# Kernel tuning notes

Measured on AMD Instinct MI355X. Metric: run time of the kernel, lower is better.

## Reference

```python
import jax, jax.numpy as jnp
import numpy as np

B, F, HU, HC = 8192, 100, 128, 512


def _lin(key, din, dout, bias=True, scale=0.02):
    k1, k2 = jax.random.split(key)
    w = jax.random.normal(k1, (din, dout), jnp.float32) * scale
    if bias:
        b = jax.random.normal(k2, (dout,), jnp.float32) * scale
        return w, b
    return (w,)


def setup_inputs() -> dict:
    key = jax.random.key(0)
    ks = jax.random.split(key, 24)
    d = {}
    d['feature_list'] = jax.random.normal(ks[0], (B, F), jnp.float32)
    d['is_treat'] = jax.random.uniform(ks[1], (B,), jnp.float32)
    d['emb'] = jax.random.normal(ks[2], (F, HU), jnp.float32) * 0.02
    d['t_w'], d['t_b'] = _lin(ks[3], 1, HU)
    d['qw'], d['qb'] = _lin(ks[4], HU, HU)
    d['kw'], d['kb'] = _lin(ks[5], HU, HU)
    d['vw'], d['vb'] = _lin(ks[6], HU, HU)
    (d['a1w'],) = _lin(ks[7], HU, HU, bias=False)
    d['a2w'], d['a2b'] = _lin(ks[8], HU, HU)
    (d['a3w'],) = _lin(ks[9], HU, 1, bias=False)
    d['c1w'], d['c1b'] = _lin(ks[10], F * HU, HC)
    d['c2w'], d['c2b'] = _lin(ks[11], HC, HC)
    d['c3w'], d['c3b'] = _lin(ks[12], HC, HC // 2)
    d['c4w'], d['c4b'] = _lin(ks[13], HC // 2, HC // 4)
    d['c5w'], d['c5b'] = _lin(ks[14], HC // 4, HC // 8)
    d['clw'], d['clb'] = _lin(ks[15], HC // 8, 1)
    d['ctw'], d['ctb'] = _lin(ks[16], HC // 8, 1)
    d['u1w'], d['u1b'] = _lin(ks[17], HU, HU)
    d['u2w'], d['u2b'] = _lin(ks[18], HU, HU // 2)
    d['u3w'], d['u3b'] = _lin(ks[19], HU // 2, HU // 4)
    d['u4w'], d['u4b'] = _lin(ks[20], HU // 4, HU // 8)
    d['tlw'], d['tlb'] = _lin(ks[21], HU // 8, 1)
    d['utw'], d['utb'] = _lin(ks[22], HU // 8, 1)
    return d


def reference(feature_list, is_treat, emb, t_w, t_b, qw, qb, kw, kb, vw, vb,
              a1w, a2w, a2b, a3w, c1w, c1b, c2w, c2b, c3w, c3b, c4w, c4b,
              c5w, c5b, clw, clb, ctw, ctb, u1w, u1b, u2w, u2b, u3w, u3b,
              u4w, u4b, tlw, tlb, utw, utb):
    elu = jax.nn.elu
    sig = jax.nn.sigmoid
    b, f = feature_list.shape
    h = emb.shape[1]
    # per-feature embedding: [B, F, H]
    x_rep = feature_list[:, :, None] * emb[None, :, :]
    # normalize over the feature axis (dim=1), as in torch.linalg.norm(dim=1)
    nx = x_rep / jnp.linalg.norm(x_rep, axis=1, keepdims=True)
    # self-attention with sigmoid-then-softmax scores
    Q = nx @ qw + qb
    K = nx @ kw + kb
    V = nx @ vw + vb
    scores = jnp.einsum('bfh,bgh->bfg', Q, K) / (h ** 0.5)
    attn_w = jax.nn.softmax(sig(scores), axis=-1)
    xx = jnp.einsum('bfg,bgh->bfh', attn_w, V).reshape(b, f * h)
    # control net tower
    c = elu(xx @ c1w + c1b)
    c = elu(c @ c2w + c2b)
    c = elu(c @ c3w + c3b)
    c = elu(c @ c4w + c4b)
    c = elu(c @ c5w + c5b)  # is_self=True
    c_logit = c @ clw + clb
    c_tau = c @ ctw + ctb
    c_prob = sig(c_logit)
    # treatment representation: Linear(1, hu) on ones -> [B, H]
    t_rep = jnp.ones((b, 1), feature_list.dtype) @ t_w.reshape(1, h) + t_b
    # interaction attention (vectorized over features)
    att = jax.nn.relu(sig(t_rep @ a1w)[:, None, :] + sig(x_rep @ a2w + a2b))
    att = (att @ a3w)[..., 0]  # [B, F]
    attn = jax.nn.softmax(att, axis=1)
    xt = jnp.einsum('bf,bfh->bh', attn, x_rep)
    # uplift net tower
    u = elu(xt @ u1w + u1b)
    u = elu(u @ u2w + u2b)
    u = elu(u @ u3w + u3b)
    u = elu(u @ u4w + u4b)  # is_self=True
    t_logit = u @ tlw + tlb
    u_tau = u @ utw + utb
    t_prob = sig(t_logit)
    return (c_logit, c_prob, c_tau, t_logit, t_prob, u_tau)
```

## Files before the change

### kernel.cpp

```cpp
#include <hip/hip_runtime.h>
#include <hip/hip_bf16.h>

typedef __bf16 bf16;
typedef __bf16 bf16x8 __attribute__((ext_vector_type(8)));
typedef __bf16 bf16x4 __attribute__((ext_vector_type(4)));
typedef float f32x4 __attribute__((ext_vector_type(4)));
typedef unsigned u32x4 __attribute__((ext_vector_type(4)));

#define DEVI static __device__ __forceinline__

DEVI float sigmoidf_(float x){ return 1.0f/(1.0f+__expf(-x)); }
DEVI float eluf_(float x){ return x>0.f ? x : (__expf(x)-1.f); }
DEVI f32x4 mfma16(bf16x8 a, bf16x8 b, f32x4 c){ return __builtin_amdgcn_mfma_f32_16x16x32_bf16(a,b,c,0,0,0); }
DEVI f32x4 mfma8(long a, long b, f32x4 c){ return __builtin_amdgcn_mfma_f32_16x16x32_fp8_fp8(a,b,c,0,0,0); }
DEVI unsigned pack2_(float a, float b){
    union { bf16 v[2]; unsigned u; } t; t.v[0]=(bf16)a; t.v[1]=(bf16)b; return t.u;
}
DEVI unsigned long long pack4_(float a, float b, float c, float d){
    union { bf16 v[4]; unsigned long long u; } t;
    t.v[0]=(bf16)a; t.v[1]=(bf16)b; t.v[2]=(bf16)c; t.v[3]=(bf16)d; return t.u;
}
DEVI unsigned cvtfp8x4_(float a, float b, float c, float d){
    int v = __builtin_amdgcn_cvt_pk_fp8_f32(a, b, 0, false);
    v = __builtin_amdgcn_cvt_pk_fp8_f32(c, d, v, true);
    return (unsigned)v;
}
DEVI void gld16_(const void* g, void* l){
    __builtin_amdgcn_global_load_lds((const __attribute__((address_space(1))) void*)g,
                                     (__attribute__((address_space(3))) void*)l, 16, 0, 0);
}

#define B_ 8192
#define F_ 100
#define FP 112
#define H_ 128
#define KC_ 12800
#define SPLIT_ 4
#define FP8SC 16.0f

#define SWZ(r,bc) ((bc) ^ (((r)&7)<<4))
DEVI int swzk_(int row, int k){ return (k & ~127) | ((k & 127) ^ ((row&7)<<4)); }

DEVI void dotrans_(float (*t)[33], const float* in, bf16* out, int R, int C, int bx, int by, int tid){
    int c0 = bx*32, r0 = by*32;
    int tc = tid & 31, tr = tid >> 5;
    #pragma unroll
    for (int i=0;i<4;i++){
        int r = tr + i*8;
        t[r][tc] = in[(size_t)(r0+r)*C + c0 + tc];
    }
    __syncthreads();
    #pragma unroll
    for (int i=0;i<4;i++){
        int ro = tr + i*8;
        out[(size_t)(c0+ro)*R + r0 + tc] = (bf16)t[tc][ro];
    }
}

DEVI void dotrans_swz_(float (*t)[33], const float* in, bf16* out, int R, int C, int bx, int by, int tid){
    int c0 = bx*32, r0 = by*32;
    int tc = tid & 31, tr = tid >> 5;
    #pragma unroll
    for (int i=0;i<4;i++){
        int r = tr + i*8;
        t[r][tc] = in[(size_t)(r0+r)*C + c0 + tc];
    }
    __syncthreads();
    #pragma unroll
    for (int i=0;i<4;i++){
        int ro = tr + i*8;
        int n = c0+ro;
        int ob = swzk_(n, (r0+tc)*2);
        *(bf16*)((char*)out + (size_t)n*R*2 + ob) = (bf16)t[tc][ro];
    }
}

__global__ void k_prep_all(const float* __restrict__ qw, const float* __restrict__ qb,
                           const float* __restrict__ kw, const float* __restrict__ kb,
                           const float* __restrict__ tw, const float* __restrict__ tb,
                           const float* __restrict__ a1w, const float* __restrict__ vw,
                           const float* __restrict__ a2w, const float* __restrict__ c2w,
                           const float* __restrict__ c3w,
                           bf16* __restrict__ mextT, float* __restrict__ sigt, float* __restrict__ cconst,
                           bf16* __restrict__ wvT, bf16* __restrict__ wa2t,
                           bf16* __restrict__ c2wt, bf16* __restrict__ c3wt){
    __shared__ float t[32][33];
    const float rsc = 0.08838834764831845f;
    int blk = blockIdx.x, tid = threadIdx.x;
    if (blk < 9){
        #pragma unroll 1
        for (int e=0; e<8; ++e){
            int idx = e*256 + tid;
            int n = blk*16 + (idx>>7), h = idx&127;
            float acc = 0.f;
            if (n < 128){
                for (int d=0; d<128; ++d) acc += qw[h*128+d]*kw[n*128+d];
            } else if (n == 128){
                for (int d=0; d<128; ++d) acc += qw[h*128+d]*kb[d];
            } else if (n == 129){
                for (int d=0; d<128; ++d) acc += kw[h*128+d]*qb[d];
            }
            mextT[n*128+h] = (bf16)(acc*rsc);
        }
    } else if (blk == 9){
        if (tid < 128){
            float acc = 0.f;
            for (int h=0; h<128; ++h) acc += (tw[h]+tb[h]) * a1w[h*128+tid];
            sigt[tid] = sigmoidf_(acc);
        } else if (tid == 128){
            float acc = 0.f;
            for (int d=0; d<128; ++d) acc += qb[d]*kb[d];
            cconst[0] = acc*rsc;
        }
    } else if (blk < 26){
        int i = blk-10; dotrans_(t, vw, wvT, 128,128, i&3, i>>2, tid);
    } else if (blk < 42){
        int i = blk-26; dotrans_(t, a2w, wa2t, 128,128, i&3, i>>2, tid);
    } else if (blk < 298){
        int i = blk-42; dotrans_swz_(t, c2w, c2wt, 512,512, i&15, i>>4, tid);
    } else {
        int i = blk-298; dotrans_swz_(t, c3w, c3wt, 512,256, i&7, i>>3, tid);
    }
}

DEVI int kappa_(int k){
    int f = k>>7, h = k&127;
    if (f < 96)
        return (((f>>4)<<3) | (h>>4))*256 + ((f&15)>>2)*64 + (h&15)*4 + (f&3);
    else
        return 12288 + (h>>4)*64 + (h&15)*4 + (f&3);
}

__global__ __launch_bounds__(256,2) void k_gk(
    const float* __restrict__ c1w, unsigned char* __restrict__ c1wtk8,
    const float* __restrict__ feat, const float* __restrict__ emb,
    const bf16* __restrict__ wa2t, const float* __restrict__ a2b,
    const float* __restrict__ a3w, const float* __restrict__ sigt,
    float* __restrict__ attg)
{
    __shared__ char A[37888];
    int blk = blockIdx.x, tid = threadIdx.x;
    if (blk < 6400){
        float (*t)[33] = (float(*)[33])A;
        const int C = 512;
        int c0 = (blk&15)*32, r0 = (blk>>4)*32;
        int tc = tid & 31, tr = tid >> 5;
        #pragma unroll
        for (int i=0;i<4;i++){
            int r = tr + i*8;
            t[r][tc] = c1w[(size_t)(r0+r)*C + c0 + tc];
        }
        __syncthreads();
        #pragma unroll
        for (int i=0;i<4;i++){
            int ro = tr + i*8;
            float x = t[tc][ro]*FP8SC;
            int v = __builtin_amdgcn_cvt_pk_fp8_f32(x, x, 0, false);
            int n = c0+ro;
            c1wtk8[(size_t)n*KC_ + swzk_(n, kappa_(r0+tc))] = (unsigned char)v;
        }
        return;
    }
    bf16 (*sAt)[72] = (bf16(*)[72])A;
    bf16 (*sBt)[72] = (bf16(*)[72])(A + 18432);
    float (*sRed)[128] = (float(*)[128])(A + 36864);
    int w=tid>>6, lane=tid&63, l15=lane&15, l4=lane>>4;
    int m0 = (blk-6400)*128;
    int wr = w>>1, wc = w&1;
    f32x4 acc[4][4];
    #pragma unroll
    for(int mi=0;mi<4;mi++)
        #pragma unroll
        for(int ni=0;ni<4;ni++) acc[mi][ni] = (f32x4){0.f,0.f,0.f,0.f};

    #pragma unroll 1
    for (int k0=0; k0<128; k0+=64){
        __syncthreads();
        #pragma unroll
        for (int t4=0; t4<4; t4++){
            int t = tid + t4*256;
            int row=t>>3, col=(t&7)*8;
            int gr = m0+row;
            int bb = gr/112, ff = gr - bb*112;
            bf16x8 o;
            if (ff < F_){
                float fv = feat[(size_t)bb*F_ + ff];
                const float* ep = emb + ff*H_ + k0 + col;
                f32x4 e0 = *(const f32x4*)ep;
                f32x4 e1 = *(const f32x4*)(ep+4);
                o[0]=(bf16)(fv*e0[0]); o[1]=(bf16)(fv*e0[1]); o[2]=(bf16)(fv*e0[2]); o[3]=(bf16)(fv*e0[3]);
                o[4]=(bf16)(fv*e1[0]); o[5]=(bf16)(fv*e1[1]); o[6]=(bf16)(fv*e1[2]); o[7]=(bf16)(fv*e1[3]);
            } else {
                #pragma unroll
                for (int e=0;e<8;e++) o[e]=(bf16)0.f;
            }
            *(bf16x8*)&sAt[row][col] = o;
            *(bf16x8*)&sBt[row][col] = *(const bf16x8*)(wa2t + row*H_ + k0 + col);
        }
        __syncthreads();
        #pragma unroll
        for(int ks=0;ks<2;ks++){
            bf16x8 af[4], bfr[4];
            #pragma unroll
            for(int mi=0;mi<4;mi++) af[mi] = *(const bf16x8*)&sAt[wr*64+mi*16+l15][ks*32+l4*8];
            #pragma unroll
            for(int ni=0;ni<4;ni++) bfr[ni] = *(const bf16x8*)&sBt[wc*64+ni*16+l15][ks*32+l4*8];
            #pragma unroll
            for(int mi=0;mi<4;mi++)
                #pragma unroll
                for(int ni=0;ni<4;ni++)
                    acc[mi][ni] = mfma16(af[mi], bfr[ni], acc[mi][ni]);
        }
    }
    float sg[4], ab[4], a3[4];
    #pragma unroll
    for (int ni=0;ni<4;ni++){
        int n = wc*64 + ni*16 + l15;
        sg[ni]=sigt[n]; ab[ni]=a2b[n]; a3[ni]=a3w[n];
    }
    #pragma unroll
    for (int mi=0;mi<4;mi++){
        float sj[4] = {0.f,0.f,0.f,0.f};
        #pragma unroll
        for (int ni=0;ni<4;ni++){
            #pragma unroll
            for (int j=0;j<4;j++){
                float u = sigmoidf_(acc[mi][ni][j] + ab[ni]);
                float t = sg[ni] + u;
                t = t>0.f ? t : 0.f;
                sj[j] += t*a3[ni];
            }
        }
        #pragma unroll
        for (int j=0;j<4;j++){
            float v = sj[j];
            #pragma unroll
            for (int m=1;m<16;m<<=1) v += __shfl_xor(v,m,16);
            sj[j]=v;
        }
        if (l15==0){
            #pragma unroll
            for (int j=0;j<4;j++) sRed[wc][wr*64+mi*16+l4*4+j] = sj[j];
        }
    }
    __syncthreads();
    if (tid < 128) attg[(size_t)m0 + tid] = sRed[0][tid] + sRed[1][tid];
}

__global__ __launch_bounds__(512,2) void k_attn2(
    const float* __restrict__ feat, const float* __restrict__ emb,
    const bf16* __restrict__ mextT, const bf16* __restrict__ wvT,
    const float* __restrict__ vb, const float* __restrict__ cconst,
    const float* __restrict__ attg,
    unsigned char* __restrict__ xxb, bf16* __restrict__ xtb)
{
    __shared__ char L[81792];
    char* Lm = L;
    char* Ln = L + 32768;
    float* sFeat  = (float*)(L+61440);
    float* normP  = (float*)(L+62336);
    float* sAw    = (float*)(L+77568);
    float* sNorm  = (float*)(L+79872);
    float* sAlpha = (float*)(L+80384);
    float* sBeta  = (float*)(L+80832);
    float* sInv   = (float*)(L+81280);

    int b = blockIdx.x;
    int tid = threadIdx.x, w = tid>>6, lane = tid&63;
    int l15 = lane&15, l4 = lane>>4;
    bf16 (*sP)[72] = (bf16(*)[72])(L + 61440 + w*2304);

    bf16x8 awv[4];
    #pragma unroll
    for (int kc=0;kc<4;kc++)
        awv[kc] = *(const bf16x8*)(wvT + (w*16+l15)*H_ + kc*32 + l4*8);
    float vbr = vb[w*16+l15];

    #pragma unroll 2
    for (int v = tid; v < 128*16; v += 512){
        int n = v >> 4, cg = (v & 15) * 8;
        *(u32x4*)(Lm + n*256 + SWZ(n, cg*2)) = *(const u32x4*)(mextT + n*128 + cg);
    }
    if (tid < FP) sFeat[tid] = (tid<F_) ? feat[(size_t)b*F_+tid] : 0.f;
    if (w==0){
        const float* ag = attg + (size_t)b*FP;
        float a0 = (lane<F_)? ag[lane] : -1e30f;
        float a1 = (lane+64<F_)? ag[lane+64] : -1e30f;
        float m = fmaxf(a0,a1);
        #pragma unroll
        for(int s=1;s<64;s<<=1) m = fmaxf(m, __shfl_xor(m,s,64));
        float e0 = (lane<F_)? __expf(a0-m):0.f;
        float e1 = (lane+64<F_)? __expf(a1-m):0.f;
        float s = e0+e1;
        #pragma unroll
        for(int t=1;t<64;t<<=1) s += __shfl_xor(s,t,64);
        float inv = 1.f/s;
        if (lane<FP) sAw[lane] = e0*inv;
        if (lane+64<FP) sAw[lane+64] = e1*inv;
    }
    __syncthreads();

    int hp = (tid&63)*2, gg = tid>>6;
    {
        float fa0=0.f, fa1=0.f;
        #pragma unroll 4
        for (int it=0; it<13; ++it){
            int f = gg + 8*it;
            if (f < F_){
                float2 e2 = *(const float2*)(emb + f*H_ + hp);
                float v0 = sFeat[f]*e2.x, v1 = sFeat[f]*e2.y;
                fa0 += v0*v0; fa1 += v1*v1;
            }
        }
        *(float2*)(normP + gg*128 + hp) = make_float2(fa0, fa1);
    }
    __syncthreads();
    if (tid < 128){
        float s = 0.f;
        #pragma unroll
        for (int g2=0; g2<8; ++g2) s += normP[g2*128 + tid];
        sNorm[tid] = sqrtf(s);
    }
    __syncthreads();

    {
        float rn0 = __builtin_amdgcn_rcpf(sNorm[hp]);
        float rn1 = __builtin_amdgcn_rcpf(sNorm[hp+1]);
        #pragma unroll 4
        for (int it=0; it<13; ++it){
            int f = gg + 8*it;
            if (f < F_){
                float2 e2 = *(const float2*)(emb + f*H_ + hp);
                *(unsigned*)(Ln + f*256 + SWZ(f, hp*2)) = pack2_(sFeat[f]*e2.x*rn0, sFeat[f]*e2.y*rn1);
            }
        }
        for (int z=tid; z<768; z+=512){
            int f = 100 + (z>>6), hz = (z&63)*2;
            *(unsigned*)(Ln + f*256 + SWZ(f, hz*2)) = 0u;
        }
    }
    __syncthreads();

    int mt = w;

    if (mt < 7){
        bf16x8 bfr8[4];
        #pragma unroll
        for (int kc=0;kc<4;kc++)
            bfr8[kc] = *(const bf16x8*)(mextT + (128+(l15&1))*H_ + kc*32 + l4*8);
        f32x4 acc = {0.f,0.f,0.f,0.f};
        #pragma unroll
        for (int kc=0;kc<4;kc++){
            bf16x8 a = *(const bf16x8*)(Ln + (mt*16+l15)*256 + SWZ(mt*16+l15, (kc*32+l4*8)*2));
            acc = mfma16(a, bfr8[kc], acc);
        }
        if (l15==0){
            #pragma unroll
            for (int j=0;j<4;j++) sAlpha[mt*16+l4*4+j] = acc[j];
        }
        if (l15==1){
            #pragma unroll
            for (int j=0;j<4;j++) sBeta[mt*16+l4*4+j] = acc[j];
        }
    }
    __syncthreads();

    const float cc = cconst[0];
    unsigned long long uexB[3];
    if (mt < 7){
        bf16x8 afxi[4];
        #pragma unroll
        for (int kc=0;kc<4;kc++)
            afxi[kc] = *(const bf16x8*)(Ln + (mt*16+l15)*256 + SWZ(mt*16+l15, (kc*32+l4*8)*2));
        f32x4 sc[7];
        #pragma unroll
        for (int gt=0; gt<7; gt++) sc[gt] = (f32x4){0.f,0.f,0.f,0.f};
        #pragma unroll 1
        for (int p=0; p<2; p++){
            #pragma unroll 2
            for (int nt4=0; nt4<4; nt4++){
                int nt = p*4 + nt4;
                bf16x8 bw[4];
                #pragma unroll
                for (int kc=0;kc<4;kc++)
                    bw[kc] = *(const bf16x8*)(Lm + (nt*16+l15)*256 + SWZ(nt*16+l15, (kc*32+l4*8)*2));
                f32x4 d = {0.f,0.f,0.f,0.f};
                #pragma unroll
                for (int kc=0;kc<4;kc++) d = mfma16(bw[kc], afxi[kc], d);
                *(unsigned long long*)(&sP[l15][nt4*16 + l4*4]) = pack4_(d[0],d[1],d[2],d[3]);
            }
            bf16x8 afs0 = *(const bf16x8*)&sP[l15][l4*8];
            bf16x8 afs1 = *(const bf16x8*)&sP[l15][32+l4*8];
            #pragma unroll
            for (int gt=0; gt<7; gt++){
                int r = gt*16+l15;
                bf16x8 b0 = *(const bf16x8*)(Ln + r*256 + SWZ(r, (p*64 + l4*8)*2));
                bf16x8 b1 = *(const bf16x8*)(Ln + r*256 + SWZ(r, (p*64 + 32 + l4*8)*2));
                sc[gt] = mfma16(b0, afs0, sc[gt]);
                sc[gt] = mfma16(b1, afs1, sc[gt]);
            }
        }
        float aj = sAlpha[mt*16+l15];
        float rs = 0.f;
        #pragma unroll
        for (int gt=0; gt<7; gt++){
            f32x4 bt4 = *(const f32x4*)&sBeta[gt*16+l4*4];
            float e[4];
            #pragma unroll
            for (int j=0;j<4;j++){
                int g = gt*16 + l4*4 + j;
                float val = sc[gt][j] + aj + bt4[j] + cc;
                e[j] = (g<F_) ? __expf(sigmoidf_(val)) : 0.f;
                rs += e[j];
            }
            if (gt < 4)
                *(unsigned long long*)(&sP[l15][gt*16 + l4*4]) = pack4_(e[0],e[1],e[2],e[3]);
            else
                uexB[gt-4] = pack4_(e[0],e[1],e[2],e[3]);
        }
        rs += __shfl_xor(rs, 16, 64);
        rs += __shfl_xor(rs, 32, 64);
        if (l4 == 0) sInv[w*16 + l15] = 1.f/rs;
    } else {
        int h = lane;
        float a0=0.f, a1=0.f;
        #pragma unroll 4
        for (int f=0; f<F_; ++f){
            float awf = sAw[f];
            a0 += awf * (float)*(const bf16*)(Ln + f*256 + SWZ(f, h*2));
            a1 += awf * (float)*(const bf16*)(Ln + f*256 + SWZ(f, (h+64)*2));
        }
        xtb[(size_t)b*H_ + h]      = (bf16)(a0 * sNorm[h]);
        xtb[(size_t)b*H_ + h + 64] = (bf16)(a1 * sNorm[h+64]);
    }

    unsigned long long vpku[7];
    #pragma unroll
    for (int gt=0; gt<7; gt++){
        f32x4 acc = {0.f,0.f,0.f,0.f};
        #pragma unroll
        for (int kc=0;kc<4;kc++){
            int r = gt*16+l15;
            bf16x8 a = *(const bf16x8*)(Ln + r*256 + SWZ(r, (kc*32+l4*8)*2));
            acc = mfma16(a, awv[kc], acc);
        }
        vpku[gt] = pack4_(acc[0]+vbr, acc[1]+vbr, acc[2]+vbr, acc[3]+vbr);
    }
    __syncthreads();

    {
        int hrow = w*16 + l15;
        #pragma unroll
        for (int gt=0; gt<7; gt++)
            *(unsigned long long*)(Lm + hrow*256 + SWZ(hrow, gt*32 + l4*8)) = vpku[gt];
    }
    __syncthreads();

    if (mt < 7){
        bf16x8 ap0 = *(const bf16x8*)&sP[l15][l4*8];
        bf16x8 ap1 = *(const bf16x8*)&sP[l15][32+l4*8];
        f32x4 acc8[8];
        #pragma unroll
        for (int ht=0;ht<8;ht++) acc8[ht] = (f32x4){0.f,0.f,0.f,0.f};
        #pragma unroll
        for (int ht=0; ht<8; ht++){
            int r = ht*16+l15;
            bf16x8 bv0 = *(const bf16x8*)(Lm + r*256 + SWZ(r, (l4*8)*2));
            bf16x8 bv1 = *(const bf16x8*)(Lm + r*256 + SWZ(r, (32+l4*8)*2));
            acc8[ht] = mfma16(ap0, bv0, acc8[ht]);
            acc8[ht] = mfma16(ap1, bv1, acc8[ht]);
        }
        #pragma unroll
        for (int gt=4; gt<7; gt++)
            *(unsigned long long*)(&sP[l15][(gt-4)*16 + l4*4]) = uexB[gt-4];
        *(unsigned long long*)(&sP[l15][48 + l4*4]) = 0ull;
        bf16x8 ap2 = *(const bf16x8*)&sP[l15][l4*8];
        bf16x8 ap3 = *(const bf16x8*)&sP[l15][32+l4*8];
        #pragma unroll
        for (int ht=0; ht<8; ht++){
            int r = ht*16+l15;
            int c2 = 64+l4*8;
            int c3 = 96+l4*8;  if (c3 >= 112) c3 = 96;
            bf16x8 bv2 = *(const bf16x8*)(Lm + r*256 + SWZ(r, c2*2));
            bf16x8 bv3 = *(const bf16x8*)(Lm + r*256 + SWZ(r, c3*2));
            acc8[ht] = mfma16(ap2, bv2, acc8[ht]);
            acc8[ht] = mfma16(ap3, bv3, acc8[ht]);
        }
        float fs[4];
        #pragma unroll
        for (int j=0;j<4;j++) fs[j] = sInv[w*16 + l4*4 + j] * FP8SC;
        #pragma unroll
        for (int ht=0; ht<8; ht++){
            unsigned u = cvtfp8x4_(acc8[ht][0]*fs[0], acc8[ht][1]*fs[1], acc8[ht][2]*fs[2], acc8[ht][3]*fs[3]);
            if (mt < 6){
                *(unsigned*)(xxb + (size_t)b*KC_ + swzk_(b, (mt*8+ht)*256 + lane*4)) = u;
            } else if (l4 == 0){
                *(unsigned*)(xxb + (size_t)b*KC_ + swzk_(b, 12288 + ht*64 + l15*4)) = u;
            }
        }
    }
}

__global__ __launch_bounds__(512,2) void k_gemm_fp8(const unsigned char* __restrict__ A,
        const unsigned char* __restrict__ Bt, bf16* __restrict__ part, int M, int N, int K, int KS)
{
    __shared__ unsigned char S[49152];
    int tid=threadIdx.x, w=tid>>6, lane=tid&63, l15=lane&15, l4=lane>>4;
    int m0 = blockIdx.y*128, n0 = blockIdx.x*256;
    int kbeg = blockIdx.z*KS, kend = kbeg + KS;
    int wr = w>>2, wc = w&3;
    int offW = w*1024 + lane*16;
    int rS = offW >> 7, cS = offW & 127;
    f32x4 acc[4][4];
    #pragma unroll
    for(int mi=0;mi<4;mi++)
        #pragma unroll
        for(int ni=0;ni<4;ni++) acc[mi][ni] = (f32x4){0.f,0.f,0.f,0.f};

    int sx = (l15&7)<<4;

    for (int k0=kbeg; k0<kend; k0+=128){
        __syncthreads();
        gld16_(A + (size_t)(m0 + rS     )*K + k0 + cS, S + offW);
        gld16_(A + (size_t)(m0 + rS + 64)*K + k0 + cS, S + offW + 8192);
        #pragma unroll
        for (int q=0;q<4;q++)
            gld16_(Bt + (size_t)(n0 + q*64 + rS)*K + k0 + cS, S + 16384 + q*8192 + offW);
        __syncthreads();
        #pragma unroll
        for(int ks=0;ks<4;ks++){
            int co = (ks*32 + l4*8) ^ sx;
            long af[4], bfr[4];
            #pragma unroll
            for(int mi=0;mi<4;mi++) af[mi] = *(const long*)(S + (wr*64+mi*16+l15)*128 + co);
            #pragma unroll
            for(int ni=0;ni<4;ni++) bfr[ni] = *(const long*)(S + 16384 + (wc*64+ni*16+l15)*128 + co);
            #pragma unroll
            for(int mi=0;mi<4;mi++)
                #pragma unroll
                for(int ni=0;ni<4;ni++)
                    acc[mi][ni] = mfma8(af[mi], bfr[ni], acc[mi][ni]);
        }
    }
    bf16* pz = part + (size_t)blockIdx.z*M*N;
    #pragma unroll
    for(int mi=0;mi<4;mi++)
        #pragma unroll
        for(int ni=0;ni<4;ni++){
            int col = n0 + wc*64 + ni*16 + l15;
            #pragma unroll
            for(int j=0;j<4;j++){
                int row = m0 + wr*64 + mi*16 + l4*4 + j;
                pz[(size_t)row*N + col] = (bf16)acc[mi][ni][j];
            }
        }
}

__global__ void k_c1fin(const bf16* __restrict__ part, const float* __restrict__ bias,
                        bf16* __restrict__ out){
    const size_t MN = (size_t)B_*512;
    size_t e0 = ((size_t)blockIdx.x*256 + threadIdx.x)*4;
    bf16x4 p0 = *(const bf16x4*)(part + e0);
    bf16x4 p1 = *(const bf16x4*)(part + MN + e0);
    bf16x4 p2 = *(const bf16x4*)(part + 2*MN + e0);
    bf16x4 p3 = *(const bf16x4*)(part + 3*MN + e0);
    f32x4 bb = *(const f32x4*)(bias + (e0 & 511));
    const float ds = 1.0f/(FP8SC*FP8SC);
    float s0 = ((float)p0[0]+(float)p1[0]+(float)p2[0]+(float)p3[0])*ds + bb[0];
    float s1 = ((float)p0[1]+(float)p1[1]+(float)p2[1]+(float)p3[1])*ds + bb[1];
    float s2 = ((float)p0[2]+(float)p1[2]+(float)p2[2]+(float)p3[2])*ds + bb[2];
    float s3 = ((float)p0[3]+(float)p1[3]+(float)p2[3]+(float)p3[3])*ds + bb[3];
    unsigned long long u = pack4_(eluf_(s0), eluf_(s1), eluf_(s2), eluf_(s3));
    int row = (int)(e0 >> 9);
    int ob = swzk_(row, (int)(e0 & 511) * 2);
    *(unsigned long long*)((char*)out + (size_t)row*1024 + ob) = u;
}

template<int BN, bool SWZOUT>
__global__ __launch_bounds__(256,2) void k_gemm_g(const bf16* __restrict__ A, const bf16* __restrict__ Bt,
        const float* __restrict__ bias, bf16* __restrict__ out, int M, int N, int K)
{
    __shared__ unsigned char S[32768 + BN*256];
    int tid=threadIdx.x, w=tid>>6, lane=tid&63, l15=lane&15, l4=lane>>4;
    int m0 = blockIdx.y*128, n0 = blockIdx.x*BN;
    constexpr int MI = (BN==128)?4:2;
    int wr = (BN==128)? (w>>1) : w;
    int wc = (BN==128)? (w&1) : 0;
    int offT = tid*16;
    int rS = offT >> 8, cS = offT & 255;
    f32x4 acc[MI][4];
    #pragma unroll
    for(int mi=0;mi<MI;mi++)
        #pragma unroll
        for(int ni=0;ni<4;ni++) acc[mi][ni] = (f32x4){0.f,0.f,0.f,0.f};

    int sx = (l15&7)<<4;

    for (int k0=0; k0<K; k0+=128){
        __syncthreads();
        #pragma unroll
        for (int q=0;q<8;q++)
            gld16_((const char*)A + ((size_t)(m0 + q*16 + rS)*K + k0)*2 + cS, S + q*4096 + offT);
        #pragma unroll
        for (int q=0;q<BN/16;q++)
            gld16_((const char*)Bt + ((size_t)(n0 + q*16 + rS)*K + k0)*2 + cS, S + 32768 + q*4096 + offT);
        __syncthreads();
        #pragma unroll
        for(int ks=0;ks<4;ks++){
            int co = (ks*32 + l4*8)*2;
            co = (co & ~127) | ((co & 127) ^ sx);
            bf16x8 af[MI], bfr[4];
            #pragma unroll
            for(int mi=0;mi<MI;mi++) af[mi] = *(const bf16x8*)(S + (wr*(MI*16)+mi*16+l15)*256 + co);
            #pragma unroll
            for(int ni=0;ni<4;ni++) bfr[ni] = *(const bf16x8*)(S + 32768 + (wc*64+ni*16+l15)*256 + co);
            #pragma unroll
            for(int mi=0;mi<MI;mi++)
                #pragma unroll
                for(int ni=0;ni<4;ni++)
                    acc[mi][ni] = mfma16(af[mi], bfr[ni], acc[mi][ni]);
        }
    }
    #pragma unroll
    for(int mi=0;mi<MI;mi++)
        #pragma unroll
        for(int ni=0;ni<4;ni++){
            int col = n0 + wc*64 + ni*16 + l15;
            float bc = bias[col];
            #pragma unroll
            for(int j=0;j<4;j++){
                int row = m0 + wr*(MI*16) + mi*16 + l4*4 + j;
                float v = eluf_(acc[mi][ni][j] + bc);
                if (SWZOUT){
                    int ob = swzk_(row, col*2);
                    *(bf16*)((char*)out + (size_t)row*N*2 + ob) = (bf16)v;
                } else {
                    out[(size_t)row*N + col] = (bf16)v;
                }
            }
        }
}

__global__ __launch_bounds__(256,2) void k_tails(const bf16* __restrict__ c3o,
    const float* __restrict__ c4w, const float* __restrict__ c4b,
    const float* __restrict__ c5w, const float* __restrict__ c5b,
    const float* __restrict__ clw, const float* __restrict__ clb,
    const float* __restrict__ ctw, const float* __restrict__ ctb,
    const bf16* __restrict__ xtb,
    const float* __restrict__ u1w, const float* __restrict__ u1b,
    const float* __restrict__ u2w, const float* __restrict__ u2b,
    const float* __restrict__ u3w, const float* __restrict__ u3b,
    const float* __restrict__ u4w, const float* __restrict__ u4b,
    const float* __restrict__ tlw, const float* __restrict__ tlb,
    const float* __restrict__ utw, const float* __restrict__ utb, float* __restrict__ outp)
{
    __shared__ char A[58880];
    int tid = threadIdx.x, blk = blockIdx.x;
    int r0 = (blk>>1)*32;
    if ((blk & 1) == 0){
        float (*sA)[260] = (float(*)[260])A;
        float (*sB)[132] = (float(*)[132])(A + 33280);
        float (*sC)[68]  = (float(*)[68])(A + 50176);
        for (int v=tid; v<32*64; v+=256){
            int r=v>>6, c=(v&63)*4;
            bf16x4 x = *(const bf16x4*)(c3o + (size_t)(r0+r)*256 + c);
            sA[r][c]=(float)x[0]; sA[r][c+1]=(float)x[1]; sA[r][c+2]=(float)x[2]; sA[r][c+3]=(float)x[3];
        }
        __syncthreads();
        {
            int j = tid&127, rb = tid>>7;
            float acc[16];
            #pragma unroll
            for (int i=0;i<16;i++) acc[i]=c4b[j];
            #pragma unroll 4
            for (int h=0;h<256;h++){
                float wv = c4w[h*128+j];
                #pragma unroll
                for (int i=0;i<16;i++) acc[i] += sA[2*i+rb][h]*wv;
            }
            #pragma unroll
            for (int i=0;i<16;i++) sB[2*i+rb][j] = eluf_(acc[i]);
        }
        __syncthreads();
        {
            int j = tid&63, rb = tid>>6;
            float acc[8];
            #pragma unroll
            for (int i=0;i<8;i++) acc[i]=c5b[j];
            #pragma unroll 4
            for (int h=0;h<128;h++){
                float wv = c5w[h*64+j];
                #pragma unroll
                for (int i=0;i<8;i++) acc[i] += sB[4*i+rb][h]*wv;
            }
            #pragma unroll
            for (int i=0;i<8;i++) sC[4*i+rb][j] = eluf_(acc[i]);
        }
        __syncthreads();
        if (tid < 32){
            float r1 = clb[0], r2 = ctb[0];
            #pragma unroll 8
            for (int k=0;k<64;k++){ float v = sC[tid][k]; r1 += v*clw[k]; r2 += v*ctw[k]; }
            int row = r0 + tid;
            outp[row] = r1;
            outp[B_ + row] = sigmoidf_(r1);
            outp[(size_t)2*B_ + row] = r2;
        }
    } else {
        float (*sA)[132] = (float(*)[132])A;
        float (*sB)[132] = (float(*)[132])(A + 16896);
        float (*sC)[68]  = (float(*)[68])(A + 33792);
        float (*sD)[36]  = (float(*)[36])(A + 42496);
        float (*sE)[20]  = (float(*)[20])(A + 47104);
        for (int v=tid; v<32*32; v+=256){
            int r=v>>5, c=(v&31)*4;
            bf16x4 x = *(const bf16x4*)(xtb + (size_t)(r0+r)*128 + c);
            sA[r][c]=(float)x[0]; sA[r][c+1]=(float)x[1]; sA[r][c+2]=(float)x[2]; sA[r][c+3]=(float)x[3];
        }
        __syncthreads();
        {
            int j = tid&127, rb = tid>>7;
            float acc[16];
            #pragma unroll
            for (int i=0;i<16;i++) acc[i]=u1b[j];
            #pragma unroll 4
            for (int h=0;h<128;h++){
                float wv = u1w[h*128+j];
                #pragma unroll
                for (int i=0;i<16;i++) acc[i] += sA[2*i+rb][h]*wv;
            }
            #pragma unroll
            for (int i=0;i<16;i++) sB[2*i+rb][j] = eluf_(acc[i]);
        }
        __syncthreads();
        {
            int j = tid&63, rb = tid>>6;
            float acc[8];
            #pragma unroll
            for (int i=0;i<8;i++) acc[i]=u2b[j];
            #pragma unroll 4
            for (int h=0;h<128;h++){
                float wv = u2w[h*64+j];
                #pragma unroll
                for (int i=0;i<8;i++) acc[i] += sB[4*i+rb][h]*wv;
            }
            #pragma unroll
            for (int i=0;i<8;i++) sC[4*i+rb][j] = eluf_(acc[i]);
        }
        __syncthreads();
        {
            int j = tid&31, rb = tid>>5;
            float acc[4];
            #pragma unroll
            for (int i=0;i<4;i++) acc[i]=u3b[j];
            #pragma unroll 4
            for (int h=0;h<64;h++){
                float wv = u3w[h*32+j];
                #pragma unroll
                for (int i=0;i<4;i++) acc[i] += sC[8*i+rb][h]*wv;
            }
            #pragma unroll
            for (int i=0;i<4;i++) sD[8*i+rb][j] = eluf_(acc[i]);
        }
        __syncthreads();
        {
            int j = tid&15, rb = tid>>4;
            float acc0=u4b[j], acc1=u4b[j];
            #pragma unroll 4
            for (int h=0;h<32;h++){
                float wv = u4w[h*16+j];
                acc0 += sD[rb][h]*wv;
                acc1 += sD[16+rb][h]*wv;
            }
            sE[rb][j] = eluf_(acc0);
            sE[16+rb][j] = eluf_(acc1);
        }
        __syncthreads();
        if (tid < 32){
            float r1 = tlb[0], r2 = utb[0];
            #pragma unroll
            for (int k=0;k<16;k++){ float v = sE[tid][k]; r1 += v*tlw[k]; r2 += v*utw[k]; }
            int row = r0 + tid;
            outp[(size_t)3*B_ + row] = r1;
            outp[(size_t)4*B_ + row] = sigmoidf_(r1);
            outp[(size_t)5*B_ + row] = r2;
        }
    }
}

extern "C" void kernel_launch(void* const* d_in, const int* in_sizes, int n_in,
                              void* d_out, int out_size, void* d_ws, size_t ws_size,
                              hipStream_t stream) {
    const float* feat=(const float*)d_in[0];
    const float* emb =(const float*)d_in[2];
    const float* t_w =(const float*)d_in[3]; const float* t_b=(const float*)d_in[4];
    const float* qw  =(const float*)d_in[5]; const float* qb =(const float*)d_in[6];
    const float* kw  =(const float*)d_in[7]; const float* kb =(const float*)d_in[8];
    const float* vw  =(const float*)d_in[9]; const float* vb =(const float*)d_in[10];
    const float* a1w =(const float*)d_in[11];
    const float* a2w =(const float*)d_in[12]; const float* a2b=(const float*)d_in[13];
    const float* a3w =(const float*)d_in[14];
    const float* c1w =(const float*)d_in[15]; const float* c1b=(const float*)d_in[16];
    const float* c2w =(const float*)d_in[17]; const float* c2b=(const float*)d_in[18];
    const float* c3w =(const float*)d_in[19]; const float* c3b=(const float*)d_in[20];
    const float* c4w =(const float*)d_in[21]; const float* c4b=(const float*)d_in[22];
    const float* c5w =(const float*)d_in[23]; const float* c5b=(const float*)d_in[24];
    const float* clw =(const float*)d_in[25]; const float* clb=(const float*)d_in[26];
    const float* ctw =(const float*)d_in[27]; const float* ctb=(const float*)d_in[28];
    const float* u1w =(const float*)d_in[29]; const float* u1b=(const float*)d_in[30];
    const float* u2w =(const float*)d_in[31]; const float* u2b=(const float*)d_in[32];
    const float* u3w =(const float*)d_in[33]; const float* u3b=(const float*)d_in[34];
    const float* u4w =(const float*)d_in[35]; const float* u4b=(const float*)d_in[36];
    const float* tlw =(const float*)d_in[37]; const float* tlb=(const float*)d_in[38];
    const float* utw =(const float*)d_in[39]; const float* utb=(const float*)d_in[40];
    float* outp = (float*)d_out;

    char* ws = (char*)d_ws;
    size_t off = 0;
    auto alloc = [&](size_t bytes)->char*{ char* p = ws + off; off += (bytes + 255) & ~(size_t)255; return p; };
    unsigned char* xxb = (unsigned char*)alloc((size_t)B_*KC_);
    bf16* part   = (bf16*)alloc((size_t)SPLIT_*B_*512*2);
    float* attg  = (float*)alloc((size_t)B_*FP*4);
    bf16* xtb    = (bf16*)alloc((size_t)B_*128*2);
    bf16* cbuf1  = (bf16*)alloc((size_t)B_*512*2);
    bf16* mextT  = (bf16*)alloc(144*128*2);
    bf16* wvT    = (bf16*)alloc(128*128*2);
    bf16* wa2t   = (bf16*)alloc(128*128*2);
    unsigned char* c1wtk8 = (unsigned char*)alloc((size_t)512*KC_);
    bf16* c2wt   = (bf16*)alloc((size_t)512*512*2);
    bf16* c3wt   = (bf16*)alloc((size_t)512*256*2);
    float* sigt  = (float*)alloc(128*4);
    float* cconst= (float*)alloc(4);
    bf16* cbuf2 = (bf16*)(xxb);
    bf16* cbuf3 = (bf16*)(xxb + (16u<<20));
    (void)ws_size; (void)in_sizes; (void)n_in; (void)out_size;

    k_prep_all<<<426,256,0,stream>>>(qw,qb,kw,kb,t_w,t_b,a1w, vw, a2w, c2w, c3w,
                                     mextT, sigt, cconst, wvT, wa2t, c2wt, c3wt);

    k_gk<<<13568,256,0,stream>>>(c1w, c1wtk8, feat, emb, wa2t, a2b, a3w, sigt, attg);

    k_attn2<<<B_,512,0,stream>>>(feat,emb,mextT,wvT,vb,cconst,attg, xxb, xtb);

    k_gemm_fp8<<<dim3(2,64,SPLIT_),512,0,stream>>>(xxb, c1wtk8, part, B_,512,KC_, KC_/SPLIT_);
    k_c1fin<<<4096,256,0,stream>>>(part, c1b, cbuf1);

    k_gemm_g<128,true><<<dim3(4,64),256,0,stream>>>(cbuf1, c2wt, c2b, cbuf2, B_,512,512);
    k_gemm_g<64,false><<<dim3(4,64),256,0,stream>>>(cbuf2, c3wt, c3b, cbuf3, B_,256,512);

    k_tails<<<512,256,0,stream>>>(cbuf3,c4w,c4b,c5w,c5b,clw,clb,ctw,ctb,
                                  xtb,u1w,u1b,u2w,u2b,u3w,u3b,u4w,u4b,tlw,tlb,utw,utb,outp);
}
```

Baseline: 597.4 us.

## Fold uplift tower into fp8 GEMM launch as extra blocks

Moves the uplift MLP tower out of the combined tail kernel and runs it as 256 extra blocks appended to the split-K fp8 GEMM grid, using a flattened block index. The control tail becomes its own smaller kernel. The aim is to overlap the independent uplift computation with the large GEMM and shorten the final serial kernel. Risks include extra work possibly spilling into a second wave of the GEMM, half-idle 512-thread blocks, and register pressure from the merged kernel.

```diff
diff --git a/kernel.cpp b/kernel.cpp
--- a/kernel.cpp
+++ b/kernel.cpp
@@ -501,13 +501,106 @@
     }
 }
 
-__global__ __launch_bounds__(512,2) void k_gemm_fp8(const unsigned char* __restrict__ A,
-        const unsigned char* __restrict__ Bt, bf16* __restrict__ part, int M, int N, int K, int KS)
+__global__ __launch_bounds__(512,2) void k_gemm_fp8u(const unsigned char* __restrict__ A,
+        const unsigned char* __restrict__ Bt, bf16* __restrict__ part, int M, int N, int K, int KS,
+        const bf16* __restrict__ xtb,
+        const float* __restrict__ u1w, const float* __restrict__ u1b,
+        const float* __restrict__ u2w, const float* __restrict__ u2b,
+        const float* __restrict__ u3w, const float* __restrict__ u3b,
+        const float* __restrict__ u4w, const float* __restrict__ u4b,
+        const float* __restrict__ tlw, const float* __restrict__ tlb,
+        const float* __restrict__ utw, const float* __restrict__ utb, float* __restrict__ outp)
 {
     __shared__ unsigned char S[49152];
-    int tid=threadIdx.x, w=tid>>6, lane=tid&63, l15=lane&15, l4=lane>>4;
-    int m0 = blockIdx.y*128, n0 = blockIdx.x*256;
-    int kbeg = blockIdx.z*KS, kend = kbeg + KS;
+    int bid = blockIdx.x, tid = threadIdx.x;
+    if (bid >= 512){
+        float (*tA)[132] = (float(*)[132])S;
+        float (*tB)[132] = (float(*)[132])(S + 16896);
+        float (*tC)[68]  = (float(*)[68])S;
+        float (*tD)[36]  = (float(*)[36])(S + 8704);
+        float (*tE)[20]  = (float(*)[20])(S + 13312);
+        int r0 = (bid - 512) * 32;
+        if (tid < 256){
+            for (int v=tid; v<32*32; v+=256){
+                int r=v>>5, c=(v&31)*4;
+                bf16x4 x = *(const bf16x4*)(xtb + (size_t)(r0+r)*128 + c);
+                tA[r][c]=(float)x[0]; tA[r][c+1]=(float)x[1]; tA[r][c+2]=(float)x[2]; tA[r][c+3]=(float)x[3];
+            }
+        }
+        __syncthreads();
+        if (tid < 256){
+            int j = tid&127, rb = tid>>7;
+            float acc[16];
+            #pragma unroll
+            for (int i=0;i<16;i++) acc[i]=u1b[j];
+            #pragma unroll 4
+            for (int h=0;h<128;h++){
+                float wv = u1w[h*128+j];
+                #pragma unroll
+                for (int i=0;i<16;i++) acc[i] += tA[2*i+rb][h]*wv;
+            }
+            #pragma unroll
+            for (int i=0;i<16;i++) tB[2*i+rb][j] = eluf_(acc[i]);
+        }
+        __syncthreads();
+        if (tid < 256){
+            int j = tid&63, rb = tid>>6;
+            float acc[8];
+            #pragma unroll
+            for (int i=0;i<8;i++) acc[i]=u2b[j];
+            #pragma unroll 4
+            for (int h=0;h<128;h++){
+                float wv = u2w[h*64+j];
+                #pragma unroll
+                for (int i=0;i<8;i++) acc[i] += tB[4*i+rb][h]*wv;
+            }
+            #pragma unroll
+            for (int i=0;i<8;i++) tC[4*i+rb][j] = eluf_(acc[i]);
+        }
+        __syncthreads();
+        if (tid < 256){
+            int j = tid&31, rb = tid>>5;
+            float acc[4];
+            #pragma unroll
+            for (int i=0;i<4;i++) acc[i]=u3b[j];
+            #pragma unroll 4
+            for (int h=0;h<64;h++){
+                float wv = u3w[h*32+j];
+                #pragma unroll
+                for (int i=0;i<4;i++) acc[i] += tC[8*i+rb][h]*wv;
+            }
+            #pragma unroll
+            for (int i=0;i<4;i++) tD[8*i+rb][j] = eluf_(acc[i]);
+        }
+        __syncthreads();
+        if (tid < 256){
+            int j = tid&15, rb = tid>>4;
+            float acc0=u4b[j], acc1=u4b[j];
+            #pragma unroll 4
+            for (int h=0;h<32;h++){
+                float wv = u4w[h*16+j];
+                acc0 += tD[rb][h]*wv;
+                acc1 += tD[16+rb][h]*wv;
+            }
+            tE[rb][j] = eluf_(acc0);
+            tE[16+rb][j] = eluf_(acc1);
+        }
+        __syncthreads();
+        if (tid < 32){
+            float r1 = tlb[0], r2 = utb[0];
+            #pragma unroll
+            for (int k=0;k<16;k++){ float v = tE[tid][k]; r1 += v*tlw[k]; r2 += v*utw[k]; }
+            int row = r0 + tid;
+            outp[(size_t)3*B_ + row] = r1;
+            outp[(size_t)4*B_ + row] = sigmoidf_(r1);
+            outp[(size_t)5*B_ + row] = r2;
+        }
+        return;
+    }
+    int bx = bid & 1, by = (bid >> 1) & 63, bz = bid >> 7;
+    int w=tid>>6, lane=tid&63, l15=lane&15, l4=lane>>4;
+    int m0 = by*128, n0 = bx*256;
+    int kbeg = bz*KS, kend = kbeg + KS;
     int wr = w>>2, wc = w&3;
     int offW = w*1024 + lane*16;
     int rS = offW >> 7, cS = offW & 127;
@@ -542,7 +635,7 @@
                     acc[mi][ni] = mfma8(af[mi], bfr[ni], acc[mi][ni]);
         }
     }
-    bf16* pz = part + (size_t)blockIdx.z*M*N;
+    bf16* pz = part + (size_t)bz*M*N;
     #pragma unroll
     for(int mi=0;mi<4;mi++)
         #pragma unroll
@@ -641,150 +734,62 @@
         }
 }
 
-__global__ __launch_bounds__(256,2) void k_tails(const bf16* __restrict__ c3o,
+__global__ __launch_bounds__(256,2) void k_ctail(const bf16* __restrict__ c3o,
     const float* __restrict__ c4w, const float* __restrict__ c4b,
     const float* __restrict__ c5w, const float* __restrict__ c5b,
     const float* __restrict__ clw, const float* __restrict__ clb,
-    const float* __restrict__ ctw, const float* __restrict__ ctb,
-    const bf16* __restrict__ xtb,
-    const float* __restrict__ u1w, const float* __restrict__ u1b,
-    const float* __restrict__ u2w, const float* __restrict__ u2b,
-    const float* __restrict__ u3w, const float* __restrict__ u3b,
-    const float* __restrict__ u4w, const float* __restrict__ u4b,
-    const float* __restrict__ tlw, const float* __restrict__ tlb,
-    const float* __restrict__ utw, const float* __restrict__ utb, float* __restrict__ outp)
+    const float* __restrict__ ctw, const float* __restrict__ ctb, float* __restrict__ outp)
 {
     __shared__ char A[58880];
-    int tid = threadIdx.x, blk = blockIdx.x;
-    int r0 = (blk>>1)*32;
-    if ((blk & 1) == 0){
-        float (*sA)[260] = (float(*)[260])A;
-        float (*sB)[132] = (float(*)[132])(A + 33280);
-        float (*sC)[68]  = (float(*)[68])(A + 50176);
-        for (int v=tid; v<32*64; v+=256){
-            int r=v>>6, c=(v&63)*4;
-            bf16x4 x = *(const bf16x4*)(c3o + (size_t)(r0+r)*256 + c);
-            sA[r][c]=(float)x[0]; sA[r][c+1]=(float)x[1]; sA[r][c+2]=(float)x[2]; sA[r][c+3]=(float)x[3];
-        }
-        __syncthreads();
-        {
-            int j = tid&127, rb = tid>>7;
-            float acc[16];
-            #pragma unroll
-            for (int i=0;i<16;i++) acc[i]=c4b[j];
-            #pragma unroll 4
-            for (int h=0;h<256;h++){
-                float wv = c4w[h*128+j];
-                #pragma unroll
-                for (int i=0;i<16;i++) acc[i] += sA[2*i+rb][h]*wv;
-            }
-            #pragma unroll
-            for (int i=0;i<16;i++) sB[2*i+rb][j] = eluf_(acc[i]);
-        }
-        __syncthreads();
-        {
-            int j = tid&63, rb = tid>>6;
-            float acc[8];
-            #pragma unroll
-            for (int i=0;i<8;i++) acc[i]=c5b[j];
-            #pragma unroll 4
-            for (int h=0;h<128;h++){
-                float wv = c5w[h*64+j];
-                #pragma unroll
-                for (int i=0;i<8;i++) acc[i] += sB[4*i+rb][h]*wv;
-            }
-            #pragma unroll
-            for (int i=0;i<8;i++) sC[4*i+rb][j] = eluf_(acc[i]);
-        }
-        __syncthreads();
-        if (tid < 32){
-            float r1 = clb[0], r2 = ctb[0];
-            #pragma unroll 8
-            for (int k=0;k<64;k++){ float v = sC[tid][k]; r1 += v*clw[k]; r2 += v*ctw[k]; }
-            int row = r0 + tid;
-            outp[row] = r1;
-            outp[B_ + row] = sigmoidf_(r1);
-            outp[(size_t)2*B_ + row] = r2;
-        }
-    } else {
-        float (*sA)[132] = (float(*)[132])A;
-        float (*sB)[132] = (float(*)[132])(A + 16896);
-        float (*sC)[68]  = (float(*)[68])(A + 33792);
-        float (*sD)[36]  = (float(*)[36])(A + 42496);
-        float (*sE)[20]  = (float(*)[20])(A + 47104);
-        for (int v=tid; v<32*32; v+=256){
-            int r=v>>5, c=(v&31)*4;
-            bf16x4 x = *(const bf16x4*)(xtb + (size_t)(r0+r)*128 + c);
-            sA[r][c]=(float)x[0]; sA[r][c+1]=(float)x[1]; sA[r][c+2]=(float)x[2]; sA[r][c+3]=(float)x[3];
-        }
-        __syncthreads();
-        {
-            int j = tid&127, rb = tid>>7;
-            float acc[16];
-            #pragma unroll
-            for (int i=0;i<16;i++) acc[i]=u1b[j];
-            #pragma unroll 4
-            for (int h=0;h<128;h++){
-                float wv = u1w[h*128+j];
-                #pragma unroll
-                for (int i=0;i<16;i++) acc[i] += sA[2*i+rb][h]*wv;
-            }
-            #pragma unroll
-            for (int i=0;i<16;i++) sB[2*i+rb][j] = eluf_(acc[i]);
-        }
-        __syncthreads();
-        {
-            int j = tid&63, rb = tid>>6;
-            float acc[8];
-            #pragma unroll
-            for (int i=0;i<8;i++) acc[i]=u2b[j];
-            #pragma unroll 4
-            for (int h=0;h<128;h++){
-                float wv = u2w[h*64+j];
-                #pragma unroll
-                for (int i=0;i<8;i++) acc[i] += sB[4*i+rb][h]*wv;
-            }
-            #pragma unroll
-            for (int i=0;i<8;i++) sC[4*i+rb][j] = eluf_(acc[i]);
-        }
-        __syncthreads();
-        {
-            int j = tid&31, rb = tid>>5;
-            float acc[4];
-            #pragma unroll
-            for (int i=0;i<4;i++) acc[i]=u3b[j];
-            #pragma unroll 4
-            for (int h=0;h<64;h++){
-                float wv = u3w[h*32+j];
-                #pragma unroll
-                for (int i=0;i<4;i++) acc[i] += sC[8*i+rb][h]*wv;
-            }
-            #pragma unroll
-            for (int i=0;i<4;i++) sD[8*i+rb][j] = eluf_(acc[i]);
-        }
-        __syncthreads();
-        {
-            int j = tid&15, rb = tid>>4;
-            float acc0=u4b[j], acc1=u4b[j];
-            #pragma unroll 4
-            for (int h=0;h<32;h++){
-                float wv = u4w[h*16+j];
-                acc0 += sD[rb][h]*wv;
-                acc1 += sD[16+rb][h]*wv;
-            }
-            sE[rb][j] = eluf_(acc0);
-            sE[16+rb][j] = eluf_(acc1);
-        }
-        __syncthreads();
-        if (tid < 32){
-            float r1 = tlb[0], r2 = utb[0];
-            #pragma unroll
-            for (int k=0;k<16;k++){ float v = sE[tid][k]; r1 += v*tlw[k]; r2 += v*utw[k]; }
-            int row = r0 + tid;
-            outp[(size_t)3*B_ + row] = r1;
-            outp[(size_t)4*B_ + row] = sigmoidf_(r1);
-            outp[(size_t)5*B_ + row] = r2;
-        }
+    float (*sA)[260] = (float(*)[260])A;
+    float (*sB)[132] = (float(*)[132])(A + 33280);
+    float (*sC)[68]  = (float(*)[68])(A + 50176);
+    int tid = threadIdx.x;
+    int r0 = blockIdx.x*32;
+    for (int v=tid; v<32*64; v+=256){
+        int r=v>>6, c=(v&63)*4;
+        bf16x4 x = *(const bf16x4*)(c3o + (size_t)(r0+r)*256 + c);
+        sA[r][c]=(float)x[0]; sA[r][c+1]=(float)x[1]; sA[r][c+2]=(float)x[2]; sA[r][c+3]=(float)x[3];
+    }
+    __syncthreads();
+    {
+        int j = tid&127, rb = tid>>7;
+        float acc[16];
+        #pragma unroll
+        for (int i=0;i<16;i++) acc[i]=c4b[j];
+        #pragma unroll 4
+        for (int h=0;h<256;h++){
+            float wv = c4w[h*128+j];
+            #pragma unroll
+            for (int i=0;i<16;i++) acc[i] += sA[2*i+rb][h]*wv;
+        }
+        #pragma unroll
+        for (int i=0;i<16;i++) sB[2*i+rb][j] = eluf_(acc[i]);
+    }
+    __syncthreads();
+    {
+        int j = tid&63, rb = tid>>6;
+        float acc[8];
+        #pragma unroll
+        for (int i=0;i<8;i++) acc[i]=c5b[j];
+        #pragma unroll 4
+        for (int h=0;h<128;h++){
+            float wv = c5w[h*64+j];
+            #pragma unroll
+            for (int i=0;i<8;i++) acc[i] += sB[4*i+rb][h]*wv;
+        }
+        #pragma unroll
+        for (int i=0;i<8;i++) sC[4*i+rb][j] = eluf_(acc[i]);
+    }
+    __syncthreads();
+    if (tid < 32){
+        float r1 = clb[0], r2 = ctb[0];
+        #pragma unroll 8
+        for (int k=0;k<64;k++){ float v = sC[tid][k]; r1 += v*clw[k]; r2 += v*ctw[k]; }
+        int row = r0 + tid;
+        outp[row] = r1;
+        outp[B_ + row] = sigmoidf_(r1);
+        outp[(size_t)2*B_ + row] = r2;
     }
 }
 
@@ -842,12 +847,12 @@
 
     k_attn2<<<B_,512,0,stream>>>(feat,emb,mextT,wvT,vb,cconst,attg, xxb, xtb);
 
-    k_gemm_fp8<<<dim3(2,64,SPLIT_),512,0,stream>>>(xxb, c1wtk8, part, B_,512,KC_, KC_/SPLIT_);
+    k_gemm_fp8u<<<768,512,0,stream>>>(xxb, c1wtk8, part, B_,512,KC_, KC_/SPLIT_,
+                                      xtb,u1w,u1b,u2w,u2b,u3w,u3b,u4w,u4b,tlw,tlb,utw,utb,outp);
     k_c1fin<<<4096,256,0,stream>>>(part, c1b, cbuf1);
 
     k_gemm_g<128,true><<<dim3(4,64),256,0,stream>>>(cbuf1, c2wt, c2b, cbuf2, B_,512,512);
     k_gemm_g<64,false><<<dim3(4,64),256,0,stream>>>(cbuf2, c3wt, c3b, cbuf3, B_,256,512);
 
-    k_tails<<<512,256,0,stream>>>(cbuf3,c4w,c4b,c5w,c5b,clw,clb,ctw,ctb,
-                                  xtb,u1w,u1b,u2w,u2b,u3w,u3b,u4w,u4b,tlw,tlb,utw,utb,outp);
-}
+    k_ctail<<<256,256,0,stream>>>(cbuf3,c4w,c4b,c5w,c5b,clw,clb,ctw,ctb,outp);
+}
```

New measurement: 612.9 us. +2.6%, slower.
